# Optimization experiments

Hardware: AMD Instinct MI355X
Metric: run time of the kernel (lower is better)

Reference implementation:

```python
import jax, jax.numpy as jnp
import numpy as np

DIM = 2048
H = 16       # num_heads
HKV = 4      # num_kv_heads
HD = DIM // H  # head_dim = 128
REP = H // HKV
ROPE_BASE = 10000.0
QK_GAIN_INIT = 1.0
B, T = 4, 2048


def rms_norm(x):
    # F.rms_norm with eps=None -> machine eps of dtype, no weight
    eps = jnp.finfo(x.dtype).eps
    return x * jax.lax.rsqrt(jnp.mean(x * x, axis=-1, keepdims=True) + eps)


def apply_rotary_emb(x, cos, sin):
    # x: [B, h, T, HD]; cos/sin: [T, HD//2]
    h = x.shape[-1] // 2
    x1, x2 = x[..., :h], x[..., h:]
    return jnp.concatenate((x1 * cos + x2 * sin, -x1 * sin + x2 * cos), axis=-1)


def setup_inputs() -> dict:
    key = jax.random.key(0)
    ks = jax.random.split(key, 6)
    kv_dim = HKV * HD
    x = jax.random.normal(ks[0], (B, T, DIM), dtype=jnp.float32)
    Wq = jax.random.normal(ks[1], (DIM, DIM), dtype=jnp.float32) * 0.02
    Wk = jax.random.normal(ks[2], (kv_dim, DIM), dtype=jnp.float32) * 0.02
    Wv = jax.random.normal(ks[3], (kv_dim, DIM), dtype=jnp.float32) * 0.02
    Wproj = jax.random.normal(ks[4], (DIM, DIM), dtype=jnp.float32) * 0.02
    q_gain = jnp.full((H,), QK_GAIN_INIT, dtype=jnp.float32)
    return {"x": x, "Wq": Wq, "Wk": Wk, "Wv": Wv, "Wproj": Wproj, "q_gain": q_gain}


def reference(x, Wq, Wk, Wv, Wproj, q_gain):
    Bs, Ts, D = x.shape
    # QKV projections (bias-free Linear: x @ W.T)
    q = (x @ Wq.T).reshape(Bs, Ts, H, HD).transpose(0, 2, 1, 3)      # [B,H,T,HD]
    k = (x @ Wk.T).reshape(Bs, Ts, HKV, HD).transpose(0, 2, 1, 3)    # [B,HKV,T,HD]
    v = (x @ Wv.T).reshape(Bs, Ts, HKV, HD).transpose(0, 2, 1, 3)
    # RMSNorm over head_dim
    q, k = rms_norm(q), rms_norm(k)
    # rotary
    inv_freq = 1.0 / (ROPE_BASE ** (jnp.arange(0, HD, 2, dtype=jnp.float32) / HD))
    t = jnp.arange(Ts, dtype=jnp.float32)
    freqs = jnp.outer(t, inv_freq)  # [T, HD//2]
    cos, sin = jnp.cos(freqs), jnp.sin(freqs)
    q = apply_rotary_emb(q, cos, sin)
    k = apply_rotary_emb(k, cos, sin)
    # per-head query gain
    q = q * q_gain[None, :, None, None]
    # GQA attention without materializing repeated K/V
    qg = q.reshape(Bs, HKV, REP, Ts, HD)
    scale = 1.0 / jnp.sqrt(jnp.asarray(HD, dtype=q.dtype))
    scores = jnp.einsum('bgrtd,bgsd->bgrts', qg, k) * scale  # [B,HKV,REP,T,T]
    causal = jnp.tril(jnp.ones((Ts, Ts), dtype=bool))
    scores = jnp.where(causal, scores, jnp.finfo(scores.dtype).min)
    attn = jax.nn.softmax(scores, axis=-1)
    y = jnp.einsum('bgrts,bgsd->bgrtd', attn, v)              # [B,HKV,REP,T,HD]
    y = y.reshape(Bs, H, Ts, HD).transpose(0, 2, 1, 3).reshape(Bs, Ts, D)
    return y @ Wproj.T
```

## Files before the change

kernel.cpp:

```cpp
#include <hip/hip_runtime.h>
#include <stdint.h>

typedef unsigned short u16;
typedef __attribute__((ext_vector_type(4))) float f32x4;
typedef __attribute__((ext_vector_type(8))) __bf16 bf16x8;
typedef __attribute__((ext_vector_type(4))) u16 u16x4;
typedef __attribute__((ext_vector_type(8))) u16 u16x8;

#define T_SEQ 2048
#define NB 4
#define NH 16
#define NKV 4
#define HDIM 128
#define PSTR 72

__device__ __forceinline__ u16 f2bf(float f) {
  __bf16 h = (__bf16)f;
  return __builtin_bit_cast(u16, h);
}
__device__ __forceinline__ float bf2f(u16 u) {
  union { uint32_t u; float f; } v; v.u = ((uint32_t)u) << 16;
  return v.f;
}
__device__ __forceinline__ void gload16(const void* g, void* l) {
  __builtin_amdgcn_global_load_lds((const __attribute__((address_space(1))) void*)g,
                                   (__attribute__((address_space(3))) void*)l, 16, 0, 0);
}
__device__ __forceinline__ f32x4 mfma16(bf16x8 a, bf16x8 b, f32x4 c) {
  return __builtin_amdgcn_mfma_f32_16x16x32_bf16(a, b, c, 0, 0, 0);
}

__global__ __launch_bounds__(256) void cvt_bf16(const float* __restrict__ in,
                                                u16* __restrict__ out, int n) {
  int idx = blockIdx.x * 256 + threadIdx.x;
  int stride = gridDim.x * 256;
  for (int i = idx * 4; i < n; i += stride * 4) {
    f32x4 v = *(const f32x4*)(in + i);
    u16x4 o;
    o[0] = f2bf(v[0]); o[1] = f2bf(v[1]); o[2] = f2bf(v[2]); o[3] = f2bf(v[3]);
    *(u16x4*)(out + i) = o;
  }
}

template <int MODE>
__global__ __launch_bounds__(256) void gemm128p3(const u16* __restrict__ A,
                                                 const u16* __restrict__ Bt,
                                                 u16* __restrict__ q_o, u16* __restrict__ k_o,
                                                 u16* __restrict__ v_o, float* __restrict__ f_o,
                                                 int K, int nx, int cpx) {
  __shared__ __align__(16) u16 As3[3 * 128 * 32];
  __shared__ __align__(16) u16 Bs3[3 * 128 * 32];
  const int tid = threadIdx.x;
  const int l = tid & 63, w = tid >> 6;
  const int l15 = l & 15, g16 = l >> 4;
  const int wr = w >> 1, wc = w & 1;

  const int oid = blockIdx.x + nx * blockIdx.y;
  const int wid = (oid & 7) * cpx + (oid >> 3);
  const int m0 = (wid / nx) * 128, n0 = (wid % nx) * 128;

  f32x4 acc[4][4] = {};

  const int row0 = tid >> 2, row1 = 64 + (tid >> 2), cc = tid & 3;
  const int sc0 = cc ^ ((row0 >> 1) & 3), sc1 = cc ^ ((row1 >> 1) & 3);
  const u16* pA0 = A + (size_t)(m0 + row0) * K + sc0 * 8;
  const u16* pA1 = A + (size_t)(m0 + row1) * K + sc1 * 8;
  const u16* pB0 = Bt + (size_t)(n0 + row0) * K + sc0 * 8;
  const u16* pB1 = Bt + (size_t)(n0 + row1) * K + sc1 * 8;

#define STAGE(buf)                                                   \
  {                                                                  \
    char* ab = (char*)As3 + (buf) * 8192 + w * 1024;                 \
    char* bb = (char*)Bs3 + (buf) * 8192 + w * 1024;                 \
    gload16(pA0, ab);                                                \
    gload16(pA1, ab + 4096);                                         \
    gload16(pB0, bb);                                                \
    gload16(pB1, bb + 4096);                                         \
    pA0 += 32; pA1 += 32; pB0 += 32; pB1 += 32;                      \
  }

#define COMPUTE(buf)                                                 \
  {                                                                  \
    const u16* AsB = As3 + (buf) * 4096;                             \
    const u16* BsB = Bs3 + (buf) * 4096;                             \
    bf16x8 af[4], bfr[4];                                            \
    _Pragma("unroll")                                                \
    for (int mt = 0; mt < 4; ++mt) {                                 \
      int arow = wr * 64 + mt * 16 + l15;                            \
      af[mt] = *(const bf16x8*)&AsB[arow * 32 +                      \
                                    ((g16 ^ ((arow >> 1) & 3)) * 8)];\
    }                                                                \
    _Pragma("unroll")                                                \
    for (int nt = 0; nt < 4; ++nt) {                                 \
      int brow = wc * 64 + nt * 16 + l15;                            \
      bfr[nt] = *(const bf16x8*)&BsB[brow * 32 +                     \
                                     ((g16 ^ ((brow >> 1) & 3)) * 8)];\
    }                                                                \
    __builtin_amdgcn_s_setprio(1);                                   \
    _Pragma("unroll")                                                \
    for (int mt = 0; mt < 4; ++mt)                                   \
      _Pragma("unroll")                                              \
      for (int nt = 0; nt < 4; ++nt)                                 \
        acc[mt][nt] = mfma16(af[mt], bfr[nt], acc[mt][nt]);          \
    __builtin_amdgcn_s_setprio(0);                                   \
  }

  const int ntiles = K >> 5;
  STAGE(0);
  STAGE(1);
  asm volatile("s_waitcnt vmcnt(4)" ::: "memory");
  __builtin_amdgcn_s_barrier();

  int cur = 0, nxt = 2;
  for (int t = 0; t < ntiles; ++t) {
    const bool more2 = (t + 2 < ntiles);
    if (more2) STAGE(nxt);
    COMPUTE(cur);
    if (t + 1 < ntiles) {
      if (more2) {
        asm volatile("s_waitcnt vmcnt(4)" ::: "memory");
      } else {
        asm volatile("s_waitcnt vmcnt(0)" ::: "memory");
      }
      __builtin_amdgcn_s_barrier();
    }
    cur = (cur == 2) ? 0 : cur + 1;
    nxt = (nxt == 2) ? 0 : nxt + 1;
  }
#undef STAGE
#undef COMPUTE

#pragma unroll
  for (int mt = 0; mt < 4; ++mt) {
#pragma unroll
    for (int r = 0; r < 4; ++r) {
      int row = m0 + wr * 64 + mt * 16 + g16 * 4 + r;
#pragma unroll
      for (int nt = 0; nt < 4; ++nt) {
        int n = n0 + wc * 64 + nt * 16 + l15;
        float val = acc[mt][nt][r];
        if (MODE == 1) {
          f_o[(size_t)row * 2048 + n] = val;
        } else {
          int b = row >> 11, t = row & (T_SEQ - 1);
          u16 bv = f2bf(val);
          if (n < 2048) {
            int h = n >> 7, d = n & 127;
            q_o[((size_t)(b * NH + h) * T_SEQ + t) * HDIM + d] = bv;
          } else if (n < 2560) {
            int n2 = n - 2048; int h = n2 >> 7, d = n2 & 127;
            k_o[((size_t)(b * NKV + h) * T_SEQ + t) * HDIM + d] = bv;
          } else {
            int n2 = n - 2560; int h = n2 >> 7, d = n2 & 127;
            v_o[((size_t)(b * NKV + h) * T_SEQ + t) * HDIM + d] = bv;
          }
        }
      }
    }
  }
}

template <int MODE>
__global__ __launch_bounds__(512, 2) void gemm256(const u16* __restrict__ A,
                                                  const u16* __restrict__ Bt,
                                                  u16* __restrict__ q_o, u16* __restrict__ k_o,
                                                  u16* __restrict__ v_o, float* __restrict__ f_o,
                                                  int K, int ntn, int cpx) {
  __shared__ __align__(16) u16 As[2][256 * 64];
  __shared__ __align__(16) u16 Bs[2][256 * 64];
  const int tid = threadIdx.x;
  const int l = tid & 63, w = tid >> 6;
  const int l16 = l & 15, g16 = l >> 4;
  const int wr = w >> 2, wc = w & 3;

  const int oid = blockIdx.x;
  const int wid = (oid & 7) * cpx + (oid >> 3);
  const int m0 = (wid / ntn) * 256, n0 = (wid % ntn) * 256;

  f32x4 acc[8][4] = {};

  const int srow = tid >> 3, scc = tid & 7;
  const u16* pA[4];
  const u16* pB[4];
#pragma unroll
  for (int j = 0; j < 4; ++j) {
    int row = j * 64 + srow;
    int cc = scc ^ (row & 7);
    pA[j] = A + (size_t)(m0 + row) * K + cc * 8;
    pB[j] = Bt + (size_t)(n0 + row) * K + cc * 8;
  }

#define STAGE(buf)                                              \
  {                                                             \
    char* ab = (char*)As[buf] + w * 1024;                       \
    char* bb = (char*)Bs[buf] + w * 1024;                       \
    _Pragma("unroll")                                           \
    for (int j = 0; j < 4; ++j) {                               \
      gload16(pA[j], ab + j * 8192);                            \
      pA[j] += 64;                                              \
    }                                                           \
    _Pragma("unroll")                                           \
    for (int j = 0; j < 4; ++j) {                               \
      gload16(pB[j], bb + j * 8192);                            \
      pB[j] += 64;                                              \
    }                                                           \
  }

  const int ntk = K >> 6;
  STAGE(0);
  __syncthreads();

  for (int t = 0; t < ntk; ++t) {
    const int buf = t & 1;
    if (t + 1 < ntk) STAGE(buf ^ 1);
#pragma unroll
    for (int ks = 0; ks < 2; ++ks) {
      bf16x8 bfr[4];
#pragma unroll
      for (int nf = 0; nf < 4; ++nf) {
        int brow = wc * 64 + nf * 16 + l16;
        int slot = (ks * 4 + g16) ^ (brow & 7);
        bfr[nf] = *(const bf16x8*)&Bs[buf][brow * 64 + slot * 8];
      }
#pragma unroll
      for (int rh = 0; rh < 2; ++rh) {
        bf16x8 af[4];
#pragma unroll
        for (int f = 0; f < 4; ++f) {
          int arow = wr * 128 + rh * 64 + f * 16 + l16;
          int slot = (ks * 4 + g16) ^ (arow & 7);
          af[f] = *(const bf16x8*)&As[buf][arow * 64 + slot * 8];
        }
        __builtin_amdgcn_s_setprio(1);
#pragma unroll
        for (int f = 0; f < 4; ++f)
#pragma unroll
          for (int nf = 0; nf < 4; ++nf)
            acc[rh * 4 + f][nf] = mfma16(af[f], bfr[nf], acc[rh * 4 + f][nf]);
        __builtin_amdgcn_s_setprio(0);
      }
    }
    __syncthreads();
  }
#undef STAGE

#pragma unroll
  for (int rf = 0; rf < 8; ++rf) {
#pragma unroll
    for (int rr = 0; rr < 4; ++rr) {
      int row = m0 + wr * 128 + rf * 16 + g16 * 4 + rr;
#pragma unroll
      for (int nf = 0; nf < 4; ++nf) {
        int n = n0 + wc * 64 + nf * 16 + l16;
        float val = acc[rf][nf][rr];
        if (MODE == 1) {
          f_o[(size_t)row * 2048 + n] = val;
        } else {
          int b = row >> 11, t = row & (T_SEQ - 1);
          u16 bv = f2bf(val);
          if (n < 2048) {
            int h = n >> 7, d = n & 127;
            q_o[((size_t)(b * NH + h) * T_SEQ + t) * HDIM + d] = bv;
          } else if (n < 2560) {
            int n2 = n - 2048; int h = n2 >> 7, d = n2 & 127;
            k_o[((size_t)(b * NKV + h) * T_SEQ + t) * HDIM + d] = bv;
          } else {
            int n2 = n - 2560; int h = n2 >> 7, d = n2 & 127;
            v_o[((size_t)(b * NKV + h) * T_SEQ + t) * HDIM + d] = bv;
          }
        }
      }
    }
  }
}

__global__ __launch_bounds__(256) void rmsrope(u16* __restrict__ buf,
                                               const float* __restrict__ gains,
                                               int nheads, float fold, int useGain) {
  const int w = threadIdx.x >> 6, l = threadIdx.x & 63;
  const int rid = blockIdx.x * 4 + w;
  const int t = rid & (T_SEQ - 1);
  const int h = (rid >> 11) % nheads;
  u16* p = buf + (size_t)rid * HDIM;
  float x1 = bf2f(p[l]), x2 = bf2f(p[l + 64]);
  float ss = x1 * x1 + x2 * x2;
#pragma unroll
  for (int m = 32; m; m >>= 1) ss += __shfl_xor(ss, m, 64);
  float rn = rsqrtf(ss * (1.0f / 128.0f) + 1.1920928955078125e-7f);
  float g = useGain ? gains[h] * fold : fold;
  float sc = rn * g;
  float inv = exp2f(-(float)l * (13.287712379549449f / 64.0f));
  float ang = (float)t * inv;
  float s, c;
  __sincosf(ang, &s, &c);
  float o1 = (x1 * c + x2 * s) * sc;
  float o2 = (x2 * c - x1 * s) * sc;
  p[l] = f2bf(o1);
  p[l + 64] = f2bf(o2);
}

__global__ __launch_bounds__(256) void vtrans(const u16* __restrict__ in,
                                              u16* __restrict__ out) {
  __shared__ u16 tileT[64][PSTR];
  const int tid = threadIdx.x;
  const int t0 = blockIdx.x * 64, d0 = blockIdx.y * 64, bg = blockIdx.z;
  const int row = tid >> 2, c0 = (tid & 3) * 16;
  const u16* src = in + ((size_t)bg * T_SEQ + t0 + row) * HDIM + d0 + c0;
  u16x8 a = *(const u16x8*)src;
  u16x8 bb = *(const u16x8*)(src + 8);
#pragma unroll
  for (int j = 0; j < 8; ++j) {
    tileT[c0 + j][row] = a[j];
    tileT[c0 + 8 + j][row] = bb[j];
  }
  __syncthreads();
  u16* dst = out + ((size_t)bg * HDIM + d0 + row) * T_SEQ + t0 + c0;
  *(u16x8*)dst = *(const u16x8*)&tileT[row][c0];
  *(u16x8*)(dst + 8) = *(const u16x8*)&tileT[row][c0 + 8];
}

__global__ __launch_bounds__(256) void attn_fwd6(const u16* __restrict__ qb,
                                                 const u16* __restrict__ kb,
                                                 const u16* __restrict__ vtb,
                                                 u16* __restrict__ yb,
                                                 const float* __restrict__ gains) {
  __shared__ __align__(16) u16 Ks[64 * 128];
  __shared__ __align__(16) u16 Vs[128 * 64];
  __shared__ __align__(16) u16 Ps[4][32 * PSTR];

  const int tid = threadIdx.x, l = tid & 63, w = tid >> 6;
  const int l16 = l & 15, g16 = l >> 4;

  const int oid = blockIdx.x + 8 * blockIdx.y;
  const int wid = (oid & 7) * 64 + (oid >> 3);
  const int pair = wid & 7, bh = wid >> 3;
  const int b = bh >> 4, h = bh & 15, gr = h >> 2;

  const float Mh = 16.33f * fabsf(gains[h]) + 0.5f;
  const u16* kbase = kb + (size_t)(b * NKV + gr) * T_SEQ * HDIM;
  const u16* vtbase = vtb + (size_t)(b * NKV + gr) * HDIM * T_SEQ;

  bf16x8 ones;
#pragma unroll
  for (int j = 0; j < 8; ++j) ones[j] = (__bf16)1.0f;

  for (int phase = 0; phase < 2; ++phase) {
    const int qt = phase ? (15 - pair) : pair;
    const int q0 = qt * 128 + w * 32;
    const int qhi = q0 + 31;

    bf16x8 qf[2][4];
    const u16* qbase = qb + ((size_t)bh * T_SEQ + q0) * HDIM;
#pragma unroll
    for (int nf = 0; nf < 2; ++nf)
#pragma unroll
      for (int s = 0; s < 4; ++s)
        qf[nf][s] = *(const bf16x8*)(qbase + (size_t)(nf * 16 + l16) * HDIM + s * 32 + g16 * 8);

    f32x4 oacc[2][8] = {};
    f32x4 dden[2] = {};
    const int ntile = 2 * qt + 2;

    for (int kt = 0; kt < ntile; ++kt) {
#pragma unroll
      for (int r = 0; r < 4; ++r) {
        int c = r * 256 + tid;
        int row = c >> 4, c16 = c & 15;
        int sc = c16 ^ (row & 7);
        gload16(kbase + ((size_t)(kt * 64 + row)) * HDIM + sc * 8,
                (char*)Ks + (r * 256 + w * 64) * 16);
      }
#pragma unroll
      for (int r = 0; r < 4; ++r) {
        int c = r * 256 + tid;
        int row = c >> 3, c8 = c & 7;
        int sc = c8 ^ (row & 7);
        gload16(vtbase + (size_t)row * T_SEQ + kt * 64 + sc * 8,
                (char*)Vs + (r * 256 + w * 64) * 16);
      }
      __syncthreads();

      if (kt * 64 <= qhi) {
        f32x4 sacc[4][2] = {};
        __builtin_amdgcn_s_setprio(1);
#pragma unroll
        for (int mt = 0; mt < 4; ++mt) {
          int key = mt * 16 + l16;
#pragma unroll
          for (int s = 0; s < 4; ++s) {
            bf16x8 kf = *(const bf16x8*)&Ks[key * 128 + ((s * 4 + g16) ^ (key & 7)) * 8];
#pragma unroll
            for (int nf = 0; nf < 2; ++nf)
              sacc[mt][nf] = mfma16(kf, qf[nf][s], sacc[mt][nf]);
          }
        }
        __builtin_amdgcn_s_setprio(0);

        const bool diagcross = (kt * 64 + 63 > q0);
#pragma unroll
        for (int mt = 0; mt < 4; ++mt) {
          int keyb = kt * 64 + mt * 16 + g16 * 4;
#pragma unroll
          for (int nf = 0; nf < 2; ++nf) {
            u16x4 p4;
#pragma unroll
            for (int r = 0; r < 4; ++r) {
              float pv = exp2f(sacc[mt][nf][r] - Mh);
              if (diagcross && (keyb + r > q0 + nf * 16 + l16)) pv = 0.f;
              p4[r] = f2bf(pv);
            }
            *(u16x4*)&Ps[w][(nf * 16 + l16) * PSTR + mt * 16 + g16 * 4] = p4;
          }
        }

        __builtin_amdgcn_s_setprio(1);
#pragma unroll
        for (int ks = 0; ks < 2; ++ks) {
          bf16x8 pa[2];
#pragma unroll
          for (int mq = 0; mq < 2; ++mq) {
            pa[mq] = *(const bf16x8*)&Ps[w][(mq * 16 + l16) * PSTR + ks * 32 + g16 * 8];
            dden[mq] = mfma16(pa[mq], ones, dden[mq]);
          }
#pragma unroll
          for (int dt = 0; dt < 8; ++dt) {
            int d = dt * 16 + l16;
            bf16x8 vv = *(const bf16x8*)&Vs[d * 64 + (((ks * 4 + g16) ^ (d & 7)) * 8)];
#pragma unroll
            for (int mq = 0; mq < 2; ++mq)
              oacc[mq][dt] = mfma16(pa[mq], vv, oacc[mq][dt]);
          }
        }
        __builtin_amdgcn_s_setprio(0);
      }
      __syncthreads();
    }

    float rden[2][4];
#pragma unroll
    for (int mq = 0; mq < 2; ++mq)
#pragma unroll
      for (int r = 0; r < 4; ++r)
        rden[mq][r] = 1.f / dden[mq][r];

#pragma unroll
    for (int mq = 0; mq < 2; ++mq)
#pragma unroll
      for (int dt = 0; dt < 8; ++dt)
#pragma unroll
        for (int r = 0; r < 4; ++r) {
          int t = q0 + mq * 16 + g16 * 4 + r;
          int d = dt * 16 + l16;
          yb[(((size_t)b * T_SEQ + t) * NH + h) * HDIM + d] = f2bf(oacc[mq][dt][r] * rden[mq][r]);
        }
    __syncthreads();
  }
}

extern "C" void kernel_launch(void* const* d_in, const int* in_sizes, int n_in,
                              void* d_out, int out_size, void* d_ws, size_t ws_size,
                              hipStream_t stream) {
  const float* x = (const float*)d_in[0];
  const float* Wq = (const float*)d_in[1];
  const float* Wk = (const float*)d_in[2];
  const float* Wv = (const float*)d_in[3];
  const float* Wproj = (const float*)d_in[4];
  const float* qg = (const float*)d_in[5];
  float* out = (float*)d_out;

  u16* xbf = (u16*)d_ws;
  u16* Wqkv = xbf + (size_t)8192 * 2048;
  u16* Wpj = Wqkv + (size_t)3072 * 2048;
  u16* qbuf = Wpj + (size_t)2048 * 2048;
  u16* kbuf = qbuf + (size_t)8192 * 2048;
  u16* vbuf = kbuf + (size_t)2048 * 2048;
  u16* ybuf = xbf;
  u16* vtbuf = Wqkv;

  cvt_bf16<<<2048, 256, 0, stream>>>(x, xbf, 8192 * 2048);
  cvt_bf16<<<2048, 256, 0, stream>>>(Wq, Wqkv, 2048 * 2048);
  cvt_bf16<<<1024, 256, 0, stream>>>(Wk, Wqkv + (size_t)2048 * 2048, 512 * 2048);
  cvt_bf16<<<1024, 256, 0, stream>>>(Wv, Wqkv + (size_t)2560 * 2048, 512 * 2048);
  cvt_bf16<<<2048, 256, 0, stream>>>(Wproj, Wpj, 2048 * 2048);

  gemm128p3<0><<<dim3(24, 64), 256, 0, stream>>>(xbf, Wqkv, qbuf, kbuf, vbuf, nullptr,
                                                 2048, 24, 192);

  rmsrope<<<32768, 256, 0, stream>>>(qbuf, qg, NH,
                                     1.4426950408889634f / 11.313708498984761f, 1);
  rmsrope<<<8192, 256, 0, stream>>>(kbuf, nullptr, NKV, 1.0f, 0);
  vtrans<<<dim3(32, 2, 16), 256, 0, stream>>>(vbuf, vtbuf);

  attn_fwd6<<<dim3(8, 64), 256, 0, stream>>>(qbuf, kbuf, vtbuf, ybuf, qg);

  gemm256<1><<<256, 512, 0, stream>>>(ybuf, Wpj, nullptr, nullptr, nullptr, out, 2048, 8, 32);
}
```

Before: 362.2 us.

## Fuse bf16 conversions into one launch and split QKV GEMM by tile size

Merges the five fp32-to-bf16 conversion launches into a single kernel that walks all tensors through one flat index range. The fused QKV projection is split in two. The Q part (N=2048) now runs on the larger 256x256 tile GEMM, and the K/V part (N=1024) runs on the 128-tile GEMM with a new mode-2 epilogue. The aim is better per-tile efficiency for the large Q GEMM and fewer launches, at the cost of one extra GEMM launch and branching inside the conversion loop.

After: 350.5 us. 3.2% less time.

```diff
diff --git a/kernel.cpp b/kernel.cpp
--- a/kernel.cpp
+++ b/kernel.cpp
@@ -30,23 +30,40 @@
   return __builtin_amdgcn_mfma_f32_16x16x32_bf16(a, b, c, 0, 0, 0);
 }
 
-__global__ __launch_bounds__(256) void cvt_bf16(const float* __restrict__ in,
-                                                u16* __restrict__ out, int n) {
+__global__ __launch_bounds__(256) void cvt_all(const float* __restrict__ x,
+                                               const float* __restrict__ wq,
+                                               const float* __restrict__ wk,
+                                               const float* __restrict__ wv,
+                                               const float* __restrict__ wp,
+                                               u16* __restrict__ xo, u16* __restrict__ wqo,
+                                               u16* __restrict__ wko, u16* __restrict__ wvo,
+                                               u16* __restrict__ wpo) {
+  const int C_X = 16777216 / 4, C_WQ = 4194304 / 4, C_WKV = 1048576 / 4;
+  const int B1 = C_X, B2 = B1 + C_WQ, B3 = B2 + C_WKV, B4 = B3 + C_WKV;
+  const int total = B4 + C_WQ;
   int idx = blockIdx.x * 256 + threadIdx.x;
   int stride = gridDim.x * 256;
-  for (int i = idx * 4; i < n; i += stride * 4) {
-    f32x4 v = *(const f32x4*)(in + i);
+  for (int c = idx; c < total; c += stride) {
+    const float* src;
+    u16* dst;
+    int off;
+    if (c < B1)      { src = x;  dst = xo;  off = c; }
+    else if (c < B2) { src = wq; dst = wqo; off = c - B1; }
+    else if (c < B3) { src = wk; dst = wko; off = c - B2; }
+    else if (c < B4) { src = wv; dst = wvo; off = c - B3; }
+    else             { src = wp; dst = wpo; off = c - B4; }
+    f32x4 v = *(const f32x4*)(src + (size_t)off * 4);
     u16x4 o;
     o[0] = f2bf(v[0]); o[1] = f2bf(v[1]); o[2] = f2bf(v[2]); o[3] = f2bf(v[3]);
-    *(u16x4*)(out + i) = o;
+    *(u16x4*)(dst + (size_t)off * 4) = o;
   }
 }
 
 template <int MODE>
 __global__ __launch_bounds__(256) void gemm128p3(const u16* __restrict__ A,
                                                  const u16* __restrict__ Bt,
-                                                 u16* __restrict__ q_o, u16* __restrict__ k_o,
-                                                 u16* __restrict__ v_o, float* __restrict__ f_o,
+                                                 u16* __restrict__ k_o, u16* __restrict__ v_o,
+                                                 float* __restrict__ f_o,
                                                  int K, int nx, int cpx) {
   __shared__ __align__(16) u16 As3[3 * 128 * 32];
   __shared__ __align__(16) u16 Bs3[3 * 128 * 32];
@@ -144,14 +161,11 @@
         } else {
           int b = row >> 11, t = row & (T_SEQ - 1);
           u16 bv = f2bf(val);
-          if (n < 2048) {
+          if (n < 512) {
             int h = n >> 7, d = n & 127;
-            q_o[((size_t)(b * NH + h) * T_SEQ + t) * HDIM + d] = bv;
-          } else if (n < 2560) {
-            int n2 = n - 2048; int h = n2 >> 7, d = n2 & 127;
             k_o[((size_t)(b * NKV + h) * T_SEQ + t) * HDIM + d] = bv;
           } else {
-            int n2 = n - 2560; int h = n2 >> 7, d = n2 & 127;
+            int n2 = n - 512; int h = n2 >> 7, d = n2 & 127;
             v_o[((size_t)(b * NKV + h) * T_SEQ + t) * HDIM + d] = bv;
           }
         }
@@ -163,8 +177,8 @@
 template <int MODE>
 __global__ __launch_bounds__(512, 2) void gemm256(const u16* __restrict__ A,
                                                   const u16* __restrict__ Bt,
-                                                  u16* __restrict__ q_o, u16* __restrict__ k_o,
-                                                  u16* __restrict__ v_o, float* __restrict__ f_o,
+                                                  u16* __restrict__ q_o,
+                                                  float* __restrict__ f_o,
                                                   int K, int ntn, int cpx) {
   __shared__ __align__(16) u16 As[2][256 * 64];
   __shared__ __align__(16) u16 Bs[2][256 * 64];
@@ -257,17 +271,8 @@
           f_o[(size_t)row * 2048 + n] = val;
         } else {
           int b = row >> 11, t = row & (T_SEQ - 1);
-          u16 bv = f2bf(val);
-          if (n < 2048) {
-            int h = n >> 7, d = n & 127;
-            q_o[((size_t)(b * NH + h) * T_SEQ + t) * HDIM + d] = bv;
-          } else if (n < 2560) {
-            int n2 = n - 2048; int h = n2 >> 7, d = n2 & 127;
-            k_o[((size_t)(b * NKV + h) * T_SEQ + t) * HDIM + d] = bv;
-          } else {
-            int n2 = n - 2560; int h = n2 >> 7, d = n2 & 127;
-            v_o[((size_t)(b * NKV + h) * T_SEQ + t) * HDIM + d] = bv;
-          }
+          int h = n >> 7, d = n & 127;
+          q_o[((size_t)(b * NH + h) * T_SEQ + t) * HDIM + d] = f2bf(val);
         }
       }
     }
@@ -477,14 +482,14 @@
   u16* ybuf = xbf;
   u16* vtbuf = Wqkv;
 
-  cvt_bf16<<<2048, 256, 0, stream>>>(x, xbf, 8192 * 2048);
-  cvt_bf16<<<2048, 256, 0, stream>>>(Wq, Wqkv, 2048 * 2048);
-  cvt_bf16<<<1024, 256, 0, stream>>>(Wk, Wqkv + (size_t)2048 * 2048, 512 * 2048);
-  cvt_bf16<<<1024, 256, 0, stream>>>(Wv, Wqkv + (size_t)2560 * 2048, 512 * 2048);
-  cvt_bf16<<<2048, 256, 0, stream>>>(Wproj, Wpj, 2048 * 2048);
-
-  gemm128p3<0><<<dim3(24, 64), 256, 0, stream>>>(xbf, Wqkv, qbuf, kbuf, vbuf, nullptr,
-                                                 2048, 24, 192);
+  cvt_all<<<2048, 256, 0, stream>>>(x, Wq, Wk, Wv, Wproj,
+                                    xbf, Wqkv, Wqkv + (size_t)2048 * 2048,
+                                    Wqkv + (size_t)2560 * 2048, Wpj);
+
+  gemm256<0><<<256, 512, 0, stream>>>(xbf, Wqkv, qbuf, nullptr, 2048, 8, 32);
+
+  gemm128p3<2><<<dim3(8, 64), 256, 0, stream>>>(xbf, Wqkv + (size_t)2048 * 2048,
+                                                kbuf, vbuf, nullptr, 2048, 8, 64);
 
   rmsrope<<<32768, 256, 0, stream>>>(qbuf, qg, NH,
                                      1.4426950408889634f / 11.313708498984761f, 1);
@@ -493,5 +498,5 @@
 
   attn_fwd6<<<dim3(8, 64), 256, 0, stream>>>(qbuf, kbuf, vtbuf, ybuf, qg);
 
-  gemm256<1><<<256, 512, 0, stream>>>(ybuf, Wpj, nullptr, nullptr, nullptr, out, 2048, 8, 32);
-}
+  gemm256<1><<<256, 512, 0, stream>>>(ybuf, Wpj, nullptr, out, 2048, 8, 32);
+}
```
